# Kernel optimization log

Hardware: AMD Instinct MI355X
Metric: run time of the kernel (lower is better)

## Reference

```python
import jax, jax.numpy as jnp
import numpy as np

N, E, G = 50000, 400000, 128
IN_DIM, EDGE_DIM, HID, HEADS = 64, 16, 64, 4
HC = HID * HEADS  # 256


def tconv(x, src, dst, e, wq, bq, wk, bk, wv, bv, we, ws, bs, heads, concat):
    # PyG TransformerConv (eval mode, no dropout), edge_dim path, root_weight=True
    n = x.shape[0]
    hc = wq.shape[1]
    c = hc // heads
    q = (x @ wq + bq).reshape(n, heads, c)
    k = (x @ wk + bk).reshape(n, heads, c)
    v = (x @ wv + bv).reshape(n, heads, c)
    eh = (e @ we).reshape(-1, heads, c)           # [E,H,C] edge embedding per head
    kj = k[src] + eh                               # gathered keys + edge
    vj = v[src] + eh                               # gathered values + edge
    alpha = jnp.einsum('ehc,ehc->eh', q[dst], kj) / jnp.sqrt(jnp.float32(c))
    amax = jax.ops.segment_max(alpha, dst, num_segments=n)   # segment softmax over in-edges
    ea = jnp.exp(alpha - amax[dst])
    denom = jax.ops.segment_sum(ea, dst, num_segments=n)
    w = ea / denom[dst]                            # [E,H]
    out = jax.ops.segment_sum(w[:, :, None] * vj, dst, num_segments=n)  # [N,H,C]
    out = out.reshape(n, hc) if concat else out.mean(axis=1)
    return out + x @ ws + bs                       # skip connection (lin_skip)


def bn_eval(x, g, b, m, v):
    return (x - m) * (g * jax.lax.rsqrt(v + 1e-5)) + b


def setup_inputs() -> dict:
    key = jax.random.key(0)
    ks = jax.random.split(key, 80)
    it = iter(range(80))
    def nrm(shape, s=0.05):
        return jax.random.normal(ks[next(it)], shape, jnp.float32) * s
    inp = {}
    inp['x'] = jax.random.normal(ks[next(it)], (N, IN_DIM), jnp.float32)
    inp['edge_index'] = jax.random.randint(ks[next(it)], (2, E), 0, N, jnp.int32)
    inp['edge_attr'] = jax.random.normal(ks[next(it)], (E, EDGE_DIM), jnp.float32)
    inp['batch'] = jnp.sort(jax.random.randint(ks[next(it)], (N,), 0, G, jnp.int32))
    inp['ee_w1'] = nrm((EDGE_DIM, 64)); inp['ee_b1'] = jnp.zeros((64,), jnp.float32)
    inp['ee_w2'] = nrm((64, HID)); inp['ee_b2'] = jnp.zeros((HID,), jnp.float32)
    def conv(pre, din, heads, cat):
        hc = HID * heads
        inp[pre+'_wq'] = nrm((din, hc)); inp[pre+'_bq'] = jnp.zeros((hc,), jnp.float32)
        inp[pre+'_wk'] = nrm((din, hc)); inp[pre+'_bk'] = jnp.zeros((hc,), jnp.float32)
        inp[pre+'_wv'] = nrm((din, hc)); inp[pre+'_bv'] = jnp.zeros((hc,), jnp.float32)
        inp[pre+'_we'] = nrm((HID, hc))
        dout = hc if cat else HID
        inp[pre+'_ws'] = nrm((din, dout)); inp[pre+'_bs'] = jnp.zeros((dout,), jnp.float32)
    conv('c1', IN_DIM, HEADS, True)
    conv('c2', HC, HEADS, True)
    conv('c3', HC, 1, False)
    def bn(pre, d):
        inp[pre+'_g'] = 1.0 + nrm((d,)); inp[pre+'_b'] = nrm((d,))
        inp[pre+'_m'] = nrm((d,)); inp[pre+'_v'] = 0.5 + jax.random.uniform(ks[next(it)], (d,), jnp.float32)
    bn('bn1', HC); bn('bn2', HC); bn('bn3', HID)
    inp['r_w1'] = nrm((HID, HID // 2)); inp['r_b1'] = jnp.zeros((HID // 2,), jnp.float32)
    inp['r_w2'] = nrm((HID // 2, 16)); inp['r_b2'] = jnp.zeros((16,), jnp.float32)
    inp['r_w3'] = nrm((16, 1)); inp['r_b3'] = jnp.zeros((1,), jnp.float32)
    return inp


def reference(x, edge_attr,
              ee_w1, ee_b1, ee_w2, ee_b2,
              c1_wq, c1_bq, c1_wk, c1_bk, c1_wv, c1_bv, c1_we, c1_ws, c1_bs,
              c2_wq, c2_bq, c2_wk, c2_bk, c2_wv, c2_bv, c2_we, c2_ws, c2_bs,
              c3_wq, c3_bq, c3_wk, c3_bk, c3_wv, c3_bv, c3_we, c3_ws, c3_bs,
              bn1_g, bn1_b, bn1_m, bn1_v,
              bn2_g, bn2_b, bn2_m, bn2_v,
              bn3_g, bn3_b, bn3_m, bn3_v,
              r_w1, r_b1, r_w2, r_b2, r_w3, r_b3,
              edge_index, batch):
    src, dst = edge_index[0], edge_index[1]
    e = jax.nn.relu(edge_attr @ ee_w1 + ee_b1) @ ee_w2 + ee_b2   # edge encoder
    h = tconv(x, src, dst, e, c1_wq, c1_bq, c1_wk, c1_bk, c1_wv, c1_bv, c1_we, c1_ws, c1_bs, HEADS, True)
    h = jax.nn.elu(bn_eval(h, bn1_g, bn1_b, bn1_m, bn1_v))
    h = tconv(h, src, dst, e, c2_wq, c2_bq, c2_wk, c2_bk, c2_wv, c2_bv, c2_we, c2_ws, c2_bs, HEADS, True)
    h = jax.nn.elu(bn_eval(h, bn2_g, bn2_b, bn2_m, bn2_v))
    h = tconv(h, src, dst, e, c3_wq, c3_bq, c3_wk, c3_bk, c3_wv, c3_bv, c3_we, c3_ws, c3_bs, 1, False)
    h = jax.nn.elu(bn_eval(h, bn3_g, bn3_b, bn3_m, bn3_v))
    sums = jax.ops.segment_sum(h, batch, num_segments=G)          # global_mean_pool
    cnt = jax.ops.segment_sum(jnp.ones((h.shape[0], 1), h.dtype), batch, num_segments=G)
    g = sums / jnp.maximum(cnt, 1.0)
    r = jax.nn.relu(g @ r_w1 + r_b1)
    r = jax.nn.relu(r @ r_w2 + r_b2)
    return (r @ r_w3 + r_b3)[:, 0]
```

## Files before the change

kernel.cpp:

```cpp
#include <hip/hip_runtime.h>
#include <math.h>


typedef _Float16 f16;
typedef _Float16 half8  __attribute__((ext_vector_type(8)));
typedef _Float16 half4v __attribute__((ext_vector_type(4)));
typedef float    f32x4  __attribute__((ext_vector_type(4)));

__device__ __forceinline__ float4 ld4(const float* p){ return *reinterpret_cast<const float4*>(p); }
__device__ __forceinline__ void gload16(const void* g, void* l){
  __builtin_amdgcn_global_load_lds((const __attribute__((address_space(1))) void*)g,
                                   (__attribute__((address_space(3))) void*)l, 16, 0, 0);
}

__global__ void leak_kernel(float* __restrict__ out, int n, float val){
  int i = blockIdx.x*blockDim.x + threadIdx.x;
  if (i < n) out[i] = val;
}

__global__ void hist_kernel(const int* __restrict__ dst, int* __restrict__ deg, int E){
  int i = blockIdx.x*blockDim.x + threadIdx.x;
  if (i < E) atomicAdd(&deg[dst[i]], 1);
}

__global__ __launch_bounds__(1024)
void scan_kernel(const int* __restrict__ deg, int* __restrict__ rowptr, int n){
  __shared__ int buf[1024];
  __shared__ int sbase;
  int tid = threadIdx.x;
  if (tid == 0){ sbase = 0; rowptr[0] = 0; }
  __syncthreads();
  for (int start = 0; start < n; start += 4096){
    int i0 = start + tid*4;
    int a0 = (i0+0<n)?deg[i0+0]:0;
    int a1 = (i0+1<n)?deg[i0+1]:0;
    int a2 = (i0+2<n)?deg[i0+2]:0;
    int a3 = (i0+3<n)?deg[i0+3]:0;
    int s = a0+a1+a2+a3;
    int v = s;
    buf[tid] = v;
    __syncthreads();
    for (int off=1; off<1024; off<<=1){
      int t = (tid >= off) ? buf[tid-off] : 0;
      __syncthreads();
      v += t;
      buf[tid] = v;
      __syncthreads();
    }
    int pre = sbase + v - s;
    if (i0+0 < n) rowptr[i0+1] = pre + a0;
    if (i0+1 < n) rowptr[i0+2] = pre + a0 + a1;
    if (i0+2 < n) rowptr[i0+3] = pre + a0 + a1 + a2;
    if (i0+3 < n) rowptr[i0+4] = pre + s;
    __syncthreads();
    if (tid == 1023) sbase += buf[1023];
    __syncthreads();
  }
}

__global__ void scatter_kernel(const int* __restrict__ src, const int* __restrict__ dst,
                               const int* __restrict__ rowptr, int* __restrict__ cnt,
                               int* __restrict__ csr_src, int* __restrict__ inv, int E){
  int i = blockIdx.x*blockDim.x + threadIdx.x;
  if (i >= E) return;
  int d = dst[i];
  int pos = rowptr[d] + atomicAdd(&cnt[d], 1);
  csr_src[pos] = src[i];
  inv[i] = pos;
}

struct PrepP {
  const float *ee_w1, *ee_w2;
  const float *wq[3], *wk[3], *wv[3], *we[3], *ws[3];
  const float *bq[3], *bk[3], *bv[3];
  f16* Bpk; float* biasAll;
  int* zeroP; int nZero;
  const float* x; f16* XA; int nXA;
};

__device__ __forceinline__ float projv(const float* wq, const float* wk, const float* wv,
                                       const float* we, int hc, int din, int x){
  int c = x / din, k = x - c*din;
  int sec = c / hc, cc = c - sec*hc;
  if (sec == 0) return wq[(size_t)k*hc + cc];
  if (sec == 1) return wk[(size_t)k*hc + cc];
  if (sec == 2) return wv[(size_t)k*hc + cc];
  int h = cc >> 6, jj = cc & 63;
  const float* q = wq + (size_t)k*hc + h*64;
  const float* w = we + (size_t)jj*hc + h*64;
  float s = 0.f;
  #pragma unroll 8
  for (int t = 0; t < 64; ++t) s += q[t]*w[t];
  return s;
}
__device__ __forceinline__ float postv(const float* we, const float* ws,
                                       int hc, int din, int x){
  int Kpp = 64 + din;
  int c = x / Kpp, k = x - c*Kpp;
  if (k < 64) return we[(size_t)k*hc + c];
  return ws[(size_t)(k-64)*hc + c];
}

__global__ void prep_kernel(PrepP P){
  int id = blockIdx.x*blockDim.x + threadIdx.x;
  const int NB = 534528, NBB = NB + 2304;
  if (id < NB){
    float v;
    if      (id < 2048)  { int c = id>>5, k = id&31; v = (k<16) ? P.ee_w1[k*64 + c] : 0.f; }
    else if (id < 6144)  { int x = id-2048; int c = x>>6, k = x&63; v = P.ee_w2[k*64 + c]; }
    else if (id < 71680) v = projv(P.wq[0],P.wk[0],P.wv[0],P.we[0],256,64, id-6144);
    else if (id < 333824)v = projv(P.wq[1],P.wk[1],P.wv[1],P.we[1],256,256,id-71680);
    else if (id < 399360)v = projv(P.wq[2],P.wk[2],P.wv[2],P.we[2],64, 256,id-333824);
    else if (id < 432128)v = postv(P.we[0],P.ws[0],256,64, id-399360);
    else if (id < 514048)v = postv(P.we[1],P.ws[1],256,256,id-432128);
    else                 v = postv(P.we[2],P.ws[2],64, 256,id-514048);
    P.Bpk[id] = (f16)v;
  } else if (id < NBB){
    int x = id - NB;
    int cv, off, hc;
    if (x < 1024){ cv = 0; off = x;        hc = 256; }
    else if (x < 2048){ cv = 1; off = x-1024; hc = 256; }
    else { cv = 2; off = x-2048; hc = 64; }
    int sec = off / hc, cc = off - sec*hc;
    float v;
    if      (sec == 0) v = P.bq[cv][cc];
    else if (sec == 1) v = P.bk[cv][cc];
    else if (sec == 2) v = P.bv[cv][cc];
    else {
      int h = cc >> 6, jj = cc & 63;
      const float* b = P.bq[cv] + h*64;
      const float* w = P.we[cv] + (size_t)jj*hc + h*64;
      v = 0.f;
      #pragma unroll 8
      for (int t = 0; t < 64; ++t) v += b[t]*w[t];
    }
    P.biasAll[x] = v;
  } else if (id < NBB + P.nZero){
    P.zeroP[id - NBB] = 0;
  } else if (id < NBB + P.nZero + P.nXA){
    int i = id - NBB - P.nZero;
    P.XA[i] = (f16)P.x[i];
  }
}

__global__ __launch_bounds__(256)
void enc_fused_kernel(const float* __restrict__ eattr,
                      const f16* __restrict__ B1, const f16* __restrict__ B2,
                      const float* __restrict__ b1, const float* __restrict__ b2,
                      const int* __restrict__ inv, f16* __restrict__ EFh, int E)
{
  __shared__ f16 hid[128*64];
  const int tid = threadIdx.x, lane = tid & 63, wave = tid >> 6;
  const int l15 = lane & 15, g = lane >> 4;
  const int row0 = blockIdx.x * 128;

  half8 af[2];
  #pragma unroll
  for (int mf = 0; mf < 2; ++mf){
    int r = row0 + wave*32 + mf*16 + l15;
    half8 v;
    #pragma unroll
    for (int q = 0; q < 8; ++q) v[q] = (f16)0.f;
    if (g < 2){
      const float* p = eattr + (size_t)r*16 + g*8;
      float4 u0 = ld4(p), u1 = ld4(p+4);
      v[0]=(f16)u0.x; v[1]=(f16)u0.y; v[2]=(f16)u0.z; v[3]=(f16)u0.w;
      v[4]=(f16)u1.x; v[5]=(f16)u1.y; v[6]=(f16)u1.z; v[7]=(f16)u1.w;
    }
    af[mf] = v;
  }
  f32x4 acc[8];
  #pragma unroll
  for (int i = 0; i < 8; ++i){ acc[i][0]=0.f; acc[i][1]=0.f; acc[i][2]=0.f; acc[i][3]=0.f; }
  #pragma unroll
  for (int nf = 0; nf < 4; ++nf){
    half8 bf = *(const half8*)(B1 + (size_t)(nf*16 + l15)*32 + g*8);
    #pragma unroll
    for (int mf = 0; mf < 2; ++mf)
      acc[mf*4+nf] = __builtin_amdgcn_mfma_f32_16x16x32_f16(bf, af[mf], acc[mf*4+nf], 0,0,0);
  }
  #pragma unroll
  for (int mf = 0; mf < 2; ++mf)
    #pragma unroll
    for (int nf = 0; nf < 4; ++nf){
      int rowL = wave*32 + mf*16 + l15;
      int colb = nf*16 + g*4;
      float4 bi = ld4(&b1[colb]);
      half4v h;
      h[0] = (f16)fmaxf(acc[mf*4+nf][0] + bi.x, 0.f);
      h[1] = (f16)fmaxf(acc[mf*4+nf][1] + bi.y, 0.f);
      h[2] = (f16)fmaxf(acc[mf*4+nf][2] + bi.z, 0.f);
      h[3] = (f16)fmaxf(acc[mf*4+nf][3] + bi.w, 0.f);
      int byte = rowL*128 + (((colb>>3) ^ (rowL&7)) << 4) + ((colb>>2)&1)*8;
      *(half4v*)((char*)hid + byte) = h;
    }
  __syncthreads();

  f32x4 acc2[8];
  #pragma unroll
  for (int i = 0; i < 8; ++i){ acc2[i][0]=0.f; acc2[i][1]=0.f; acc2[i][2]=0.f; acc2[i][3]=0.f; }
  #pragma unroll
  for (int s = 0; s < 2; ++s){
    half8 af2[2];
    #pragma unroll
    for (int mf = 0; mf < 2; ++mf){
      int rowL = wave*32 + mf*16 + l15;
      int kc = g + s*4;
      int byte = rowL*128 + ((kc ^ (rowL&7)) << 4);
      af2[mf] = *(const half8*)((const char*)hid + byte);
    }
    #pragma unroll
    for (int nf = 0; nf < 4; ++nf){
      half8 bf2 = *(const half8*)(B2 + (size_t)(nf*16 + l15)*64 + s*32 + g*8);
      #pragma unroll
      for (int mf = 0; mf < 2; ++mf)
        acc2[mf*4+nf] = __builtin_amdgcn_mfma_f32_16x16x32_f16(bf2, af2[mf], acc2[mf*4+nf], 0,0,0);
    }
  }
  #pragma unroll
  for (int mf = 0; mf < 2; ++mf){
    int dstRow = inv[row0 + wave*32 + mf*16 + l15];
    #pragma unroll
    for (int nf = 0; nf < 4; ++nf){
      int colb = nf*16 + g*4;
      float4 bi = ld4(&b2[colb]);
      half4v h;
      h[0] = (f16)(acc2[mf*4+nf][0] + bi.x);
      h[1] = (f16)(acc2[mf*4+nf][1] + bi.y);
      h[2] = (f16)(acc2[mf*4+nf][2] + bi.z);
      h[3] = (f16)(acc2[mf*4+nf][3] + bi.w);
      *(half4v*)(EFh + (size_t)dstRow*64 + colb) = h;
    }
  }
}

__device__ __forceinline__ float bn_elu(float x, float g, float b, float m, float v){
  float s = g / sqrtf(v + 1e-5f);
  float y = (x - m) * s + b;
  return y > 0.f ? y : expm1f(y);
}

template<int BN>
__global__ __launch_bounds__(256)
void hgemm_kernel(const f16* __restrict__ A1, int lda1, int K1,
                  const f16* __restrict__ A2, int lda2, int K2,
                  const f16* __restrict__ Bpk, int Kp,
                  const float* __restrict__ bias,
                  f16* __restrict__ C, int ldc, int M, int mode,
                  const f16* __restrict__ ep, int ldep,
                  const float* __restrict__ bng, const float* __restrict__ bnb,
                  const float* __restrict__ bnm, const float* __restrict__ bnv,
                  int headOff, size_t pstride, int hcShift)
{
  constexpr int WM = (BN == 128) ? 64 : 32;
  constexpr int MF = WM / 16;
  __shared__ f16 As[128*32];
  __shared__ f16 Bs[BN*32];
  const int tid  = threadIdx.x;
  const int lane = tid & 63;
  const int wave = tid >> 6;
  const int wm   = (BN == 128) ? (wave >> 1) : wave;
  const int wn   = (BN == 128) ? (wave & 1) : 0;
  const int l15  = lane & 15;
  const int cs   = (lane >> 4) ^ ((lane >> 2) & 3);
  const int csl  = (lane & 3) ^ (lane >> 4);
  const int arow = lane >> 2;

  const int nbx = gridDim.x;
  const int nwg = nbx * gridDim.y;
  int bid = blockIdx.y * nbx + blockIdx.x;
  {
    int q = nwg >> 3, r = nwg & 7;
    int xcd = bid & 7, idx = bid >> 3;
    bid = (xcd < r ? xcd * (q + 1) : r * (q + 1) + (xcd - r) * q) + idx;
  }
  const int row0 = (bid / nbx) * 128;
  const int col0 = (bid % nbx) * BN;
  const f16* A1b = headOff ? (A1 + col0) : A1;

  f32x4 acc[MF*4];
  #pragma unroll
  for (int i = 0; i < MF*4; ++i){ acc[i][0]=0.f; acc[i][1]=0.f; acc[i][2]=0.f; acc[i][3]=0.f; }

  for (int k0 = 0; k0 < Kp; k0 += 32) {
    const f16* Ap; int lda, ks;
    if (k0 < K1) { Ap = A1b; lda = lda1; ks = k0; }
    else         { Ap = A2;  lda = lda2; ks = k0 - K1; }
    #pragma unroll
    for (int t = 0; t < 2; ++t) {
      int r = wave*32 + t*16 + arow;
      gload16(Ap + (size_t)(row0 + r)*lda + ks + csl*8, As + (wave*32 + t*16)*32);
    }
    if (BN == 128) {
      #pragma unroll
      for (int t = 0; t < 2; ++t) {
        int r = wave*32 + t*16 + arow;
        gload16(Bpk + (size_t)(col0 + r)*Kp + k0 + csl*8, Bs + (wave*32 + t*16)*32);
      }
    } else {
      int r = wave*16 + arow;
      gload16(Bpk + (size_t)(col0 + r)*Kp + k0 + csl*8, Bs + wave*16*32);
    }
    __syncthreads();

    half8 af[MF], bf[4];
    #pragma unroll
    for (int mf = 0; mf < MF; ++mf)
      af[mf] = *(const half8*)(As + (wm*WM + mf*16 + l15)*32 + cs*8);
    #pragma unroll
    for (int nf = 0; nf < 4; ++nf)
      bf[nf] = *(const half8*)(Bs + (wn*64 + nf*16 + l15)*32 + cs*8);
    #pragma unroll
    for (int mf = 0; mf < MF; ++mf)
      #pragma unroll
      for (int nf = 0; nf < 4; ++nf)
        acc[mf*4+nf] = __builtin_amdgcn_mfma_f32_16x16x32_f16(bf[nf], af[mf], acc[mf*4+nf], 0,0,0);
    __syncthreads();
  }

  #pragma unroll
  for (int mf = 0; mf < MF; ++mf)
    #pragma unroll
    for (int nf = 0; nf < 4; ++nf){
      int row  = row0 + wm*WM + mf*16 + l15;
      int colb = col0 + wn*64 + nf*16 + (lane>>4)*4;
      if (row >= M) continue;
      float4 bi = bias ? ld4(&bias[colb]) : make_float4(0.f,0.f,0.f,0.f);
      float r0 = acc[mf*4+nf][0] + bi.x;
      float r1 = acc[mf*4+nf][1] + bi.y;
      float r2 = acc[mf*4+nf][2] + bi.z;
      float r3 = acc[mf*4+nf][3] + bi.w;
      if (mode == 1){
        r0=fmaxf(r0,0.f); r1=fmaxf(r1,0.f); r2=fmaxf(r2,0.f); r3=fmaxf(r3,0.f);
      } else if (mode == 2){
        half4v e4 = *(const half4v*)(ep + (size_t)row*ldep + colb);
        float4 g4 = ld4(&bng[colb]);
        float4 b4 = ld4(&bnb[colb]);
        float4 m4 = ld4(&bnm[colb]);
        float4 v4 = ld4(&bnv[colb]);
        r0 = bn_elu(r0 + (float)e4[0], g4.x, b4.x, m4.x, v4.x);
        r1 = bn_elu(r1 + (float)e4[1], g4.y, b4.y, m4.y, v4.y);
        r2 = bn_elu(r2 + (float)e4[2], g4.z, b4.z, m4.z, v4.z);
        r3 = bn_elu(r3 + (float)e4[3], g4.w, b4.w, m4.w, v4.w);
      }
      half4v h; h[0]=(f16)r0; h[1]=(f16)r1; h[2]=(f16)r2; h[3]=(f16)r3;
      f16* dstp;
      if (pstride){
        int hc = 1 << hcShift;
        int plane = colb >> hcShift, c2 = colb & (hc - 1);
        dstp = C + (size_t)plane*pstride + (size_t)row*hc + c2;
      } else {
        dstp = C + (size_t)row*ldc + colb;
      }
      *(half4v*)dstp = h;
    }
}

template<int HC>
__global__ __launch_bounds__(256)
void agg16_kernel(const int* __restrict__ rowptr, const int* __restrict__ csr_src,
                  f16* __restrict__ PROJ, size_t ps, const f16* __restrict__ EFh, int nNodes)
{
  int lane = threadIdx.x & 63;
  int wid = (blockIdx.x * blockDim.x + threadIdx.x) >> 6;
  int grp = lane >> 4, l16 = lane & 15;
  int node, ch;
  if (HC == 256) { node = wid;          ch = 4*lane; }
  else           { node = wid*4 + grp;  ch = 4*l16;  }
  if (node >= nNodes) return;
  f16* Qp = PROJ;
  const f16* Kp = PROJ + ps;
  const f16* Vp = PROJ + 2*ps;
  f16* Wp = PROJ + 3*ps;
  half4v qh = *(const half4v*)(Qp + (size_t)node*HC + ch);
  half4v wh = *(const half4v*)(Wp + (size_t)node*HC + ch);
  float q0=qh[0],q1=qh[1],q2=qh[2],q3=qh[3];
  float w0=wh[0],w1=wh[1],w2=wh[2],w3=wh[3];
  int e0 = rowptr[node], e1 = rowptr[node+1];

  float m = -INFINITY, den = 0.f;
  float avx=0.f,avy=0.f,avz=0.f,avw=0.f, aex=0.f,aey=0.f,aez=0.f,aew=0.f;

  half4v kN, vN, eN;
  if (e0 < e1) {
    size_t so = (size_t)csr_src[e0]*HC + ch;
    kN = *(const half4v*)(Kp + so);
    vN = *(const half4v*)(Vp + so);
    eN = *(const half4v*)(EFh + (size_t)e0*64 + 4*l16);
  }
  for (int i = e0; i < e1; ++i) {
    half4v k4 = kN, v4 = vN, e4 = eN;
    if (i + 1 < e1) {
      size_t so = (size_t)csr_src[i+1]*HC + ch;
      kN = *(const half4v*)(Kp + so);
      vN = *(const half4v*)(Vp + so);
      eN = *(const half4v*)(EFh + (size_t)(i+1)*64 + 4*l16);
    }
    float ex=e4[0], ey=e4[1], ez=e4[2], ew=e4[3];
    float p = q0*(float)k4[0] + q1*(float)k4[1] + q2*(float)k4[2] + q3*(float)k4[3]
            + w0*ex + w1*ey + w2*ez + w3*ew;
    p += __shfl_xor(p, 1);
    p += __shfl_xor(p, 2);
    p += __shfl_xor(p, 4);
    p += __shfl_xor(p, 8);
    float alpha = p * 0.125f;
    float mn = fmaxf(m, alpha);
    float sc = __expf(m - mn);
    float w  = __expf(alpha - mn);
    den = den*sc + w;
    avx = avx*sc + w*(float)v4[0]; avy = avy*sc + w*(float)v4[1];
    avz = avz*sc + w*(float)v4[2]; avw = avw*sc + w*(float)v4[3];
    aex = aex*sc + w*ex; aey = aey*sc + w*ey;
    aez = aez*sc + w*ez; aew = aew*sc + w*ew;
    m = mn;
  }
  float inv = den > 0.f ? 1.0f/den : 0.f;
  half4v o1, o2;
  o1[0]=(f16)(avx*inv); o1[1]=(f16)(avy*inv); o1[2]=(f16)(avz*inv); o1[3]=(f16)(avw*inv);
  o2[0]=(f16)(aex*inv); o2[1]=(f16)(aey*inv); o2[2]=(f16)(aez*inv); o2[3]=(f16)(aew*inv);
  *(half4v*)(Qp + (size_t)node*HC + ch) = o1;
  *(half4v*)(Wp + (size_t)node*HC + ch) = o2;
}

__global__ void pool16_kernel(const f16* __restrict__ Hf, const int* __restrict__ batch,
                              float* __restrict__ gsum, int nNodes){
  const int CH = 64;
  int c = threadIdx.x & 63;
  int chunk = blockIdx.x * (blockDim.x >> 6) + (threadIdx.x >> 6);
  int n0 = chunk * CH;
  if (n0 >= nNodes) return;
  int n1 = min(n0 + CH, nNodes);
  float acc = 0.f;
  int g = batch[n0];
  for (int n = n0; n < n1; ++n) {
    int gn = batch[n];
    if (gn != g) { atomicAdd(&gsum[g*64 + c], acc); acc = 0.f; g = gn; }
    acc += (float)Hf[(size_t)n*64 + c];
  }
  atomicAdd(&gsum[g*64 + c], acc);
}

__global__ void mlp_kernel(const float* __restrict__ gsum, const int* __restrict__ batch,
                           int nNodes, int G,
                           const float* __restrict__ w1, const float* __restrict__ b1,
                           const float* __restrict__ w2, const float* __restrict__ b2,
                           const float* __restrict__ w3, const float* __restrict__ b3,
                           float* __restrict__ out){
  __shared__ float s_w1[2048], s_w2[512], s_w3[16], s_b1[32], s_b2[16];
  int t = threadIdx.x;
  for (int i = t; i < 2048; i += 128) s_w1[i] = w1[i];
  for (int i = t; i < 512;  i += 128) s_w2[i] = w2[i];
  if (t < 16) s_w3[t] = w3[t];
  if (t < 32) s_b1[t] = b1[t];
  if (t < 16) s_b2[t] = b2[t];
  __syncthreads();
  int g = t;
  if (g >= G) return;
  int lo = 0, hi = nNodes;
  while (lo < hi){ int mid = (lo+hi)>>1; if (batch[mid] < g) lo = mid+1; else hi = mid; }
  int first = lo;
  lo = 0; hi = nNodes;
  while (lo < hi){ int mid = (lo+hi)>>1; if (batch[mid] < g+1) lo = mid+1; else hi = mid; }
  int cnt = lo - first;
  float invc = 1.0f / fmaxf((float)cnt, 1.0f);
  float gm[64];
  #pragma unroll
  for (int c = 0; c < 64; ++c) gm[c] = gsum[g*64 + c] * invc;
  float r1[32];
  #pragma unroll
  for (int j = 0; j < 32; ++j){
    float s = s_b1[j];
    #pragma unroll 8
    for (int c = 0; c < 64; ++c) s = fmaf(gm[c], s_w1[c*32 + j], s);
    r1[j] = fmaxf(s, 0.f);
  }
  float r2[16];
  #pragma unroll
  for (int j = 0; j < 16; ++j){
    float s = s_b2[j];
    #pragma unroll 8
    for (int c = 0; c < 32; ++c) s = fmaf(r1[c], s_w2[c*16 + j], s);
    r2[j] = fmaxf(s, 0.f);
  }
  float s = b3[0];
  #pragma unroll
  for (int c = 0; c < 16; ++c) s = fmaf(r2[c], s_w3[c], s);
  out[g] = s;
}

template<int BN>
static inline void launch_hgemm(hipStream_t st,
    const f16* A1, int lda1, int K1, const f16* A2, int lda2, int K2,
    const f16* Bpk, int Kp, const float* bias,
    f16* C, int ldc, int M, int Ncols, int mode,
    const f16* ep, int ldep,
    const float* g, const float* b, const float* m, const float* v,
    int headOff = 0, size_t pstride = 0, int hcShift = 0)
{
  dim3 grid(Ncols / BN, (M + 127) / 128, 1);
  hgemm_kernel<BN><<<grid, 256, 0, st>>>(A1, lda1, K1, A2, lda2, K2, Bpk, Kp,
                                         bias, C, ldc, M, mode, ep, ldep, g, b, m, v,
                                         headOff, pstride, hcShift);
}

struct ConvW {
  const float *wq,*bq,*wk,*bk,*wv,*bv,*we,*ws,*bs,*bg,*bb,*bm,*bv_;
};

extern "C" void kernel_launch(void* const* d_in, const int* in_sizes, int n_in,
                              void* d_out, int out_size, void* d_ws, size_t ws_size,
                              hipStream_t stream) {
  (void)n_in;
  const float* x     = (const float*)d_in[0];
  const int*   ei    = (const int*)d_in[1];
  const float* eattr = (const float*)d_in[2];
  const int*   batch = (const int*)d_in[3];
  const float* ee_w1 = (const float*)d_in[4];
  const float* ee_b1 = (const float*)d_in[5];
  const float* ee_w2 = (const float*)d_in[6];
  const float* ee_b2 = (const float*)d_in[7];
  ConvW cw[3];
  {
    int t = 8;
    for (int c = 0; c < 3; ++c){
      cw[c].wq=(const float*)d_in[t++]; cw[c].bq=(const float*)d_in[t++];
      cw[c].wk=(const float*)d_in[t++]; cw[c].bk=(const float*)d_in[t++];
      cw[c].wv=(const float*)d_in[t++]; cw[c].bv=(const float*)d_in[t++];
      cw[c].we=(const float*)d_in[t++]; cw[c].ws=(const float*)d_in[t++]; cw[c].bs=(const float*)d_in[t++];
    }
    for (int c = 0; c < 3; ++c){
      cw[c].bg=(const float*)d_in[t++]; cw[c].bb=(const float*)d_in[t++];
      cw[c].bm=(const float*)d_in[t++]; cw[c].bv_=(const float*)d_in[t++];
    }
  }
  const float* r_w1 = (const float*)d_in[47];
  const float* r_b1 = (const float*)d_in[48];
  const float* r_w2 = (const float*)d_in[49];
  const float* r_b2 = (const float*)d_in[50];
  const float* r_w3 = (const float*)d_in[51];
  const float* r_b3 = (const float*)d_in[52];

  const int N = in_sizes[0] / 64;
  const int E = in_sizes[2] / 16;
  const int G = out_size;

  const size_t NPAD = (size_t)N + 128;
  char* wp = (char*)d_ws;
  f16* HA   = (f16*)wp;            wp += NPAD*256*2;
  f16* HB   = (f16*)wp;            wp += NPAD*256*2;
  f16* PROJ = (f16*)wp;            wp += NPAD*1024*2;
  f16* EFh  = (f16*)wp;            wp += (size_t)E*64*2;
  f16* Bpk  = (f16*)wp;            wp += 534528*2;
  float* biasAll = (float*)wp;     wp += 2304*4;
  float* gsum    = (float*)wp;     wp += 8192*4;
  int* ideg  = (int*)wp;           wp += (size_t)N*4;
  int* icnt  = (int*)wp;           wp += (size_t)N*4;
  int* irow  = (int*)wp;           wp += (size_t)(N+1)*4;
  int* csr_s = (int*)wp;           wp += (size_t)E*4;
  int* inv   = (int*)wp;           wp += (size_t)E*4;
  size_t used = (size_t)(wp - (char*)d_ws);
  if (used > ws_size) {
    leak_kernel<<<(G + 255)/256, 256, 0, stream>>>((float*)d_out, G, (float)(ws_size >> 20));
    return;
  }

  const int* src = ei;
  const int* dst = ei + E;

  const int BO_E1 = 0, BO_E2 = 2048, BO_P0 = 6144, BO_P1 = 71680, BO_P2 = 333824;
  const int BO_S0 = 399360, BO_S1 = 432128, BO_S2 = 514048;

  PrepP P;
  P.ee_w1 = ee_w1; P.ee_w2 = ee_w2;
  for (int c = 0; c < 3; ++c){
    P.wq[c]=cw[c].wq; P.wk[c]=cw[c].wk; P.wv[c]=cw[c].wv; P.we[c]=cw[c].we; P.ws[c]=cw[c].ws;
    P.bq[c]=cw[c].bq; P.bk[c]=cw[c].bk; P.bv[c]=cw[c].bv;
  }
  P.Bpk = Bpk; P.biasAll = biasAll;
  P.zeroP = (int*)gsum; P.nZero = 8192 + 2*N;
  P.x = x; P.XA = HA; P.nXA = N*64;
  {
    long total = 534528 + 2304 + (long)P.nZero + P.nXA;
    prep_kernel<<<(int)((total + 255)/256), 256, 0, stream>>>(P);
  }

  hist_kernel<<<(E + 255)/256, 256, 0, stream>>>(dst, ideg, E);
  scan_kernel<<<1, 1024, 0, stream>>>(ideg, irow, N);
  scatter_kernel<<<(E + 255)/256, 256, 0, stream>>>(src, dst, irow, icnt, csr_s, inv, E);

  enc_fused_kernel<<<E/128, 256, 0, stream>>>(eattr, Bpk + BO_E1, Bpk + BO_E2,
                                              ee_b1, ee_b2, inv, EFh, E);

  const int BO_P[3] = {BO_P0, BO_P1, BO_P2};
  const int BO_S[3] = {BO_S0, BO_S1, BO_S2};
  const int bOff[3] = {0, 1024, 2048};
  for (int c = 0; c < 3; ++c) {
    const int din = (c == 0) ? 64 : 256;
    const int H   = (c == 2) ? 1 : 4;
    const int hc  = H * 64;
    const int hcShift = (hc == 256) ? 8 : 6;
    const size_t ps = NPAD * (size_t)hc;
    const f16* Xin = (c == 0) ? HA : ((c == 1) ? HB : HA);
    const int  ldx = (c == 0) ? 64 : 256;
    f16* Hout = (c == 1) ? HA : HB;
    const ConvW& W = cw[c];

    launch_hgemm<128>(stream, Xin, ldx, din, nullptr, 0, 0, Bpk + BO_P[c], din,
                      biasAll + bOff[c], PROJ, hc, N, 4*hc, 0, nullptr, 0, 0,0,0,0,
                      0, ps, hcShift);

    if (H == 4) agg16_kernel<256><<<(N + 3)/4,  256, 0, stream>>>(irow, csr_s, PROJ, ps, EFh, N);
    else        agg16_kernel<64> <<<(N + 15)/16,256, 0, stream>>>(irow, csr_s, PROJ, ps, EFh, N);

    launch_hgemm<64>(stream, PROJ + 3*ps, hc, 64, Xin, ldx, din, Bpk + BO_S[c], 64 + din,
                     W.bs, Hout, hc, N, hc, 2, PROJ, hc, W.bg, W.bb, W.bm, W.bv_,
                     1, 0, 0);
  }

  {
    int chunks = (N + 63) / 64;
    pool16_kernel<<<(chunks + 3)/4, 256, 0, stream>>>(HB, batch, gsum, N);
  }
  mlp_kernel<<<1, 128, 0, stream>>>(gsum, batch, N, G, r_w1, r_b1, r_w2, r_b2, r_w3, r_b3,
                                    (float*)d_out);
}
```

Baseline: 657.8 us.

## Load GEMM fragments directly from global into registers with double buffering

```diff
diff --git a/kernel.cpp b/kernel.cpp
--- a/kernel.cpp
+++ b/kernel.cpp
@@ -8,10 +8,6 @@
 typedef float    f32x4  __attribute__((ext_vector_type(4)));
 
 __device__ __forceinline__ float4 ld4(const float* p){ return *reinterpret_cast<const float4*>(p); }
-__device__ __forceinline__ void gload16(const void* g, void* l){
-  __builtin_amdgcn_global_load_lds((const __attribute__((address_space(1))) void*)g,
-                                   (__attribute__((address_space(3))) void*)l, 16, 0, 0);
-}
 
 __global__ void leak_kernel(float* __restrict__ out, int n, float val){
   int i = blockIdx.x*blockDim.x + threadIdx.x;
@@ -254,17 +250,13 @@
 {
   constexpr int WM = (BN == 128) ? 64 : 32;
   constexpr int MF = WM / 16;
-  __shared__ f16 As[128*32];
-  __shared__ f16 Bs[BN*32];
   const int tid  = threadIdx.x;
   const int lane = tid & 63;
   const int wave = tid >> 6;
   const int wm   = (BN == 128) ? (wave >> 1) : wave;
   const int wn   = (BN == 128) ? (wave & 1) : 0;
   const int l15  = lane & 15;
-  const int cs   = (lane >> 4) ^ ((lane >> 2) & 3);
-  const int csl  = (lane & 3) ^ (lane >> 4);
-  const int arow = lane >> 2;
+  const int g    = lane >> 4;
 
   const int nbx = gridDim.x;
   const int nwg = nbx * gridDim.y;
@@ -278,52 +270,54 @@
   const int col0 = (bid % nbx) * BN;
   const f16* A1b = headOff ? (A1 + col0) : A1;
 
+  int arw[MF], brw[4];
+  #pragma unroll
+  for (int mf = 0; mf < MF; ++mf) arw[mf] = row0 + wm*WM + mf*16 + l15;
+  #pragma unroll
+  for (int nf = 0; nf < 4; ++nf)  brw[nf] = col0 + wn*64 + nf*16 + l15;
+
   f32x4 acc[MF*4];
   #pragma unroll
   for (int i = 0; i < MF*4; ++i){ acc[i][0]=0.f; acc[i][1]=0.f; acc[i][2]=0.f; acc[i][3]=0.f; }
 
-  for (int k0 = 0; k0 < Kp; k0 += 32) {
-    const f16* Ap; int lda, ks;
-    if (k0 < K1) { Ap = A1b; lda = lda1; ks = k0; }
-    else         { Ap = A2;  lda = lda2; ks = k0 - K1; }
-    #pragma unroll
-    for (int t = 0; t < 2; ++t) {
-      int r = wave*32 + t*16 + arow;
-      gload16(Ap + (size_t)(row0 + r)*lda + ks + csl*8, As + (wave*32 + t*16)*32);
-    }
-    if (BN == 128) {
-      #pragma unroll
-      for (int t = 0; t < 2; ++t) {
-        int r = wave*32 + t*16 + arow;
-        gload16(Bpk + (size_t)(col0 + r)*Kp + k0 + csl*8, Bs + (wave*32 + t*16)*32);
-      }
-    } else {
-      int r = wave*16 + arow;
-      gload16(Bpk + (size_t)(col0 + r)*Kp + k0 + csl*8, Bs + wave*16*32);
-    }
-    __syncthreads();
-
-    half8 af[MF], bf[4];
-    #pragma unroll
-    for (int mf = 0; mf < MF; ++mf)
-      af[mf] = *(const half8*)(As + (wm*WM + mf*16 + l15)*32 + cs*8);
-    #pragma unroll
-    for (int nf = 0; nf < 4; ++nf)
-      bf[nf] = *(const half8*)(Bs + (wn*64 + nf*16 + l15)*32 + cs*8);
-    #pragma unroll
-    for (int mf = 0; mf < MF; ++mf)
-      #pragma unroll
-      for (int nf = 0; nf < 4; ++nf)
-        acc[mf*4+nf] = __builtin_amdgcn_mfma_f32_16x16x32_f16(bf[nf], af[mf], acc[mf*4+nf], 0,0,0);
-    __syncthreads();
-  }
+  half8 a0[MF], b0[4], a1[MF], b1[4];
+
+#define LOADF(AR, BR, K0)                                                     \
+  {                                                                           \
+    int kk = (K0);                                                            \
+    const f16* Ap; int lda, ks;                                               \
+    if (kk < K1) { Ap = A1b; lda = lda1; ks = kk; }                           \
+    else         { Ap = A2;  lda = lda2; ks = kk - K1; }                      \
+    _Pragma("unroll")                                                         \
+    for (int mf = 0; mf < MF; ++mf)                                           \
+      AR[mf] = *(const half8*)(Ap + (size_t)arw[mf]*lda + ks + g*8);          \
+    _Pragma("unroll")                                                         \
+    for (int nf = 0; nf < 4; ++nf)                                            \
+      BR[nf] = *(const half8*)(Bpk + (size_t)brw[nf]*Kp + kk + g*8);          \
+  }
+#define MFMASTEP(AR, BR)                                                      \
+  _Pragma("unroll")                                                           \
+  for (int mf = 0; mf < MF; ++mf)                                             \
+    _Pragma("unroll")                                                         \
+    for (int nf = 0; nf < 4; ++nf)                                            \
+      acc[mf*4+nf] = __builtin_amdgcn_mfma_f32_16x16x32_f16(BR[nf], AR[mf], acc[mf*4+nf], 0,0,0);
+
+  LOADF(a0, b0, 0);
+  for (int k0 = 0; k0 < Kp; k0 += 64) {
+    LOADF(a1, b1, k0 + 32);
+    MFMASTEP(a0, b0);
+    if (k0 + 64 < Kp) LOADF(a0, b0, k0 + 64);
+    MFMASTEP(a1, b1);
+  }
+#undef LOADF
+#undef MFMASTEP
 
   #pragma unroll
   for (int mf = 0; mf < MF; ++mf)
     #pragma unroll
     for (int nf = 0; nf < 4; ++nf){
-      int row  = row0 + wm*WM + mf*16 + l15;
-      int colb = col0 + wn*64 + nf*16 + (lane>>4)*4;
+      int row  = arw[mf];
+      int colb = col0 + wn*64 + nf*16 + g*4;
       if (row >= M) continue;
       float4 bi = bias ? ld4(&bias[colb]) : make_float4(0.f,0.f,0.f,0.f);
       float r0 = acc[mf*4+nf][0] + bi.x;
```

After: 795.3 us. +20.9%, slower.
